# Kernel tuning notes

Hardware: AMD Instinct MI355X
Metric: run time of the kernel (lower is better)

## Reference

```python
import jax, jax.numpy as jnp
import numpy as np

BATCH, SEQ = 4, 2048
D_MODEL, INNER, STATE, K, FFN = 384, 768, 16, 4, 1024


def setup_inputs() -> dict:
    key = jax.random.key(0)
    ks = jax.random.split(key, 12)
    def g(k, shape, scale=0.02):
        return jax.random.normal(k, shape, jnp.float32) * scale
    return {
        "x": jax.random.normal(ks[0], (BATCH, SEQ, D_MODEL), jnp.float32),
        "rms1_w": jnp.ones((D_MODEL,), jnp.float32),
        "rms2_w": jnp.ones((D_MODEL,), jnp.float32),
        "in_proj_w": g(ks[1], (D_MODEL, 2 * INNER)),
        "conv_w": g(ks[2], (K, INNER, INNER)),
        "conv_b": jnp.zeros((INNER,), jnp.float32),
        "x_proj_w": g(ks[3], (INNER, 2 * STATE)),
        "dt_proj_w": g(ks[4], (INNER, INNER)),
        "dt_proj_b": jnp.zeros((INNER,), jnp.float32),
        "A_log": jnp.log(jax.random.uniform(ks[5], (INNER, STATE), jnp.float32, 1.0, 16.0)),
        "D_param": jnp.ones((INNER,), jnp.float32),
        "out_proj_w": g(ks[6], (INNER, D_MODEL)),
        "ln_gamma": jnp.ones((D_MODEL,), jnp.float32),
        "ln_beta": jnp.zeros((D_MODEL,), jnp.float32),
        "gate_w": g(ks[7], (D_MODEL, FFN)),
        "up_w": g(ks[8], (D_MODEL, FFN)),
        "down_w": g(ks[9], (FFN, D_MODEL)),
    }


def rms_norm(x, w, eps=1e-6):
    norm = jnp.sqrt(jnp.mean(jnp.square(x), axis=-1, keepdims=True) + eps)
    return x / norm * w


def layer_norm(x, gamma, beta, eps=1e-5):
    mu = jnp.mean(x, axis=-1, keepdims=True)
    var = jnp.mean(jnp.square(x - mu), axis=-1, keepdims=True)
    return (x - mu) / jnp.sqrt(var + eps) * gamma + beta


def selective_scan(x, delta, A_log, Bm, Cm, Dp):
    # x, delta: [B,L,Di]; Bm, Cm: [B,L,N]; A_log: [Di,N]; Dp: [Di]
    delta = jax.nn.softplus(delta)
    A = -jnp.exp(A_log)                          # [Di,N]
    A_disc = jnp.exp(delta[..., None] * A)       # [B,L,Di,N]
    B_disc = delta[..., None] * Bm[:, :, None, :]  # [B,L,Di,N]
    xs = jnp.moveaxis(x, 1, 0)       # [L,B,Di]
    As = jnp.moveaxis(A_disc, 1, 0)  # [L,B,Di,N]
    Bs = jnp.moveaxis(B_disc, 1, 0)  # [L,B,Di,N]
    Cs = jnp.moveaxis(Cm, 1, 0)      # [L,B,N]
    h0 = jnp.zeros((x.shape[0], A_log.shape[0], A_log.shape[1]), x.dtype)
    def step(h, inp):
        x_t, A_t, B_t, C_t = inp
        h = A_t * h + B_t * x_t[..., None]          # [B,Di,N]
        y_t = jnp.einsum('bdn,bn->bd', h, C_t)      # [B,Di]
        return h, y_t
    _, ys = jax.lax.scan(step, h0, (xs, As, Bs, Cs))
    y = jnp.moveaxis(ys, 0, 1)       # [B,L,Di]
    return y + Dp * x


def mamba_core(h, in_proj_w, conv_w, conv_b, x_proj_w, dt_proj_w, dt_proj_b,
               A_log, D_param, out_proj_w, ln_gamma, ln_beta):
    xz = h @ in_proj_w                             # [B,L,2*Di]
    x_inner, z = jnp.split(xz, 2, axis=-1)
    # Conv1D SAME padding (k=4 -> pad (1,2)), channels-last, kernel [W,I,O]
    x_conv = jax.lax.conv_general_dilated(
        x_inner, conv_w, window_strides=(1,), padding='SAME',
        dimension_numbers=('NWC', 'WIO', 'NWC')) + conv_b
    x_conv = jax.nn.silu(x_conv)
    Bm, Cm = jnp.split(x_conv @ x_proj_w, 2, axis=-1)  # each [B,L,N]
    delta = x_conv @ dt_proj_w + dt_proj_b            # [B,L,Di]
    y = selective_scan(x_conv, delta, A_log, Bm, Cm, D_param)
    y = y * jax.nn.silu(z)
    out = y @ out_proj_w
    return layer_norm(out, ln_gamma, ln_beta)


def reference(x, rms1_w, rms2_w, in_proj_w, conv_w, conv_b, x_proj_w,
              dt_proj_w, dt_proj_b, A_log, D_param, out_proj_w, ln_gamma,
              ln_beta, gate_w, up_w, down_w):
    residual = x
    h = rms_norm(x, rms1_w)
    h = mamba_core(h, in_proj_w, conv_w, conv_b, x_proj_w, dt_proj_w,
                   dt_proj_b, A_log, D_param, out_proj_w, ln_gamma, ln_beta)
    x = residual + h  # dropout inactive (training=False)
    residual = x
    h = rms_norm(x, rms2_w)
    hidden = jax.nn.silu(h @ gate_w) * (h @ up_w)
    x = residual + hidden @ down_w
    return x
```

## Files before the change

kernel.cpp:

```cpp
#include <hip/hip_runtime.h>
#include <hip/hip_bf16.h>


using u16 = unsigned short;
using u32 = unsigned int;
using short8 = __attribute__((ext_vector_type(8))) short;
using f32x4  = __attribute__((ext_vector_type(4))) float;

#define TTOK 8192
#define DM 384
#define DI 768
#define NST 16
#define LSEQ 2048
#define NCH 64
#define LCH 32

#define SWZ_R(row, quad) \
  ((row) * 32 + ((((quad) ^ (row) ^ ((row) >> 2)) & 3) * 8))
#define SWZ_W(tid) SWZ_R((tid) >> 2, (tid) & 3)

__device__ __forceinline__ float bf2f(u16 a) {
  u32 u = ((u32)a) << 16;
  float f; __builtin_memcpy(&f, &u, 4); return f;
}
__device__ __forceinline__ u16 f2bf(float f) {
  u32 u; __builtin_memcpy(&u, &f, 4);
  u32 r = (u + 0x7fffu + ((u >> 16) & 1u)) >> 16;
  return (u16)r;
}
__device__ __forceinline__ int probe_bf(const void* rw) {
  return (((const u32*)rw)[0] == 0x3F803F80u) ? 1 : 0;
}
__device__ __forceinline__ float ld_in(const void* p, int i, int isbf) {
  return isbf ? bf2f(((const u16*)p)[i]) : ((const float*)p)[i];
}
__device__ __forceinline__ float fexp2(float x) {
#if __has_builtin(__builtin_amdgcn_exp2f)
  return __builtin_amdgcn_exp2f(x);
#else
  return exp2f(x);
#endif
}
__device__ __forceinline__ float wave_sum(float v) {
#pragma unroll
  for (int off = 32; off > 0; off >>= 1) v += __shfl_xor(v, off, 64);
  return v;
}

__global__ __launch_bounds__(256) void k_prep(
    const void* __restrict__ in_proj, const void* __restrict__ conv_w,
    const void* __restrict__ dt_w, const void* __restrict__ x_proj,
    const void* __restrict__ out_proj, const void* __restrict__ gate_w,
    const void* __restrict__ up_w, const void* __restrict__ down_w,
    const void* __restrict__ A_log, const void* __restrict__ conv_b,
    const void* __restrict__ dt_b, const void* __restrict__ Dp,
    const void* __restrict__ rms1_w, const void* __restrict__ rms2_w,
    const void* __restrict__ gamma, const void* __restrict__ beta,
    u16* __restrict__ W1T, u16* __restrict__ WCT, u16* __restrict__ W45T,
    u16* __restrict__ W5T, u16* __restrict__ W6T, u16* __restrict__ W7T,
    float* __restrict__ An2T, u16* __restrict__ vecs,
    u16* __restrict__ WinX, u16* __restrict__ h1pad) {
  const int isbf = probe_bf(rms1_w);
  int idx = blockIdx.x * 256 + threadIdx.x;
#define XPOSE(base, n, src, dst, R, C)                         \
  if (idx < (base) + (n)) {                                    \
    int lo = idx - (base);                                     \
    int r = lo / (C), c = lo % (C);                            \
    dst[(size_t)c * (R) + r] = f2bf(ld_in(src, lo, isbf));     \
    return;                                                    \
  }
  XPOSE(0,       589824,  in_proj,  W1T, 384, 1536)
  if (idx < 2949120) {
    int lo = idx - 589824;
    int t = lo / 589824, rem = lo % 589824;
    int j = rem / 768, n = rem % 768;
    WCT[(size_t)t * 589824 + n * 768 + j] = f2bf(ld_in(conv_w, lo, isbf));
    return;
  }
  XPOSE(2949120, 589824,  dt_w,     W45T, 768, 768)
  XPOSE(3538944, 24576,   x_proj,  (W45T + (size_t)768 * 768), 768, 32)
  XPOSE(3563520, 294912,  out_proj, W5T, 768, 384)
  XPOSE(3858432, 393216,  gate_w,   W6T, 384, 1024)
  XPOSE(4251648, 393216,  up_w,    (W6T + (size_t)1024 * 384), 384, 1024)
  XPOSE(4644864, 393216,  down_w,   W7T, 1024, 384)
#undef XPOSE
  if (idx < 5332992) {
    int lo = idx - 5038080;
    int i = lo / 768, j = lo % 768;
    WinX[lo] = f2bf(ld_in(in_proj, i * 1536 + j, isbf));
    return;
  }
  if (idx < 5345280) {
    int lo = idx - 5332992;
    int d = lo >> 4, n = lo & 15;
    An2T[n * DI + d] = -__expf(ld_in(A_log, lo, isbf)) * 1.44269504f;
    return;
  }
  if (idx < 5349120) {
    int lo = idx - 5345280;
    const void* s; int o;
    if      (lo < 768)  { s = conv_b; o = lo; }
    else if (lo < 1536) { s = dt_b;   o = lo - 768; }
    else if (lo < 2304) { s = Dp;     o = lo - 1536; }
    else if (lo < 2688) { s = rms1_w; o = lo - 2304; }
    else if (lo < 3072) { s = rms2_w; o = lo - 2688; }
    else if (lo < 3456) { s = gamma;  o = lo - 3072; }
    else                { s = beta;   o = lo - 3456; }
    vecs[lo] = f2bf(ld_in(s, o, isbf));
    return;
  }
  if (idx < 5353728) {
    int lo = idx - 5349120;
    int b = lo / (3 * DM), rem = lo % (3 * DM);
    int which = rem / DM, i = rem % DM;
    int row = b * 2051 + (which == 0 ? 0 : (2048 + which));
    h1pad[(size_t)row * DM + i] = 0;
  }
}

#define V_CB 0
#define V_DB 768
#define V_DP 1536
#define V_R1 2304
#define V_R2 2688
#define V_GA 3072
#define V_BE 3456

__global__ __launch_bounds__(128) void k_rms1(const void* __restrict__ x,
                                              const void* __restrict__ rw,
                                              const u16* __restrict__ vecs,
                                              u16* __restrict__ h1pad) {
  const int isbf = probe_bf(rw);
  int t = blockIdx.x, tid = threadIdx.x;
  int lane = tid & 63, wid = tid >> 6;
  float v[3]; float q = 0.f;
#pragma unroll
  for (int j = 0; j < 3; ++j) {
    v[j] = ld_in(x, t * DM + tid + j * 128, isbf);
    q += v[j] * v[j];
  }
  q = wave_sum(q);
  __shared__ float rq[2];
  if (lane == 0) rq[wid] = q;
  __syncthreads();
  float rr = rsqrtf((rq[0] + rq[1]) * (1.f / DM) + 1e-6f);
  int b = t >> 11, l = t & 2047;
  size_t orow = ((size_t)(b * 2051 + l + 1)) * DM;
#pragma unroll
  for (int j = 0; j < 3; ++j) {
    int i = tid + j * 128;
    h1pad[orow + i] = f2bf(v[j] * rr * bf2f(vecs[V_R1 + i]));
  }
}

__global__ __launch_bounds__(128) void k_lnrms(const float* __restrict__ outm,
                                               const void* __restrict__ xin,
                                               const void* __restrict__ rw,
                                               const u16* __restrict__ vecs,
                                               float* __restrict__ x2f,
                                               u16* __restrict__ h2) {
  const int isbf = probe_bf(rw);
  int t = blockIdx.x, tid = threadIdx.x;
  int lane = tid & 63, wid = tid >> 6;
  float v[3]; float s = 0.f, q = 0.f;
#pragma unroll
  for (int j = 0; j < 3; ++j) {
    v[j] = outm[(size_t)t * DM + tid + j * 128];
    s += v[j]; q += v[j] * v[j];
  }
  s = wave_sum(s); q = wave_sum(q);
  __shared__ float rs[2], rq[2], r2[2];
  if (lane == 0) { rs[wid] = s; rq[wid] = q; }
  __syncthreads();
  float mu = (rs[0] + rs[1]) * (1.f / DM);
  float var = (rq[0] + rq[1]) * (1.f / DM) - mu * mu;
  float rstd = rsqrtf(var + 1e-5f);
  float x2v[3]; float q2 = 0.f;
#pragma unroll
  for (int j = 0; j < 3; ++j) {
    int i = tid + j * 128;
    float ln = (v[j] - mu) * rstd * bf2f(vecs[V_GA + i]) + bf2f(vecs[V_BE + i]);
    x2v[j] = ld_in(xin, t * DM + i, isbf) + ln;
    x2f[(size_t)t * DM + i] = x2v[j];
    q2 += x2v[j] * x2v[j];
  }
  q2 = wave_sum(q2);
  if (lane == 0) r2[wid] = q2;
  __syncthreads();
  float rr = rsqrtf((r2[0] + r2[1]) * (1.f / DM) + 1e-6f);
#pragma unroll
  for (int j = 0; j < 3; ++j) {
    int i = tid + j * 128;
    h2[(size_t)t * DM + i] = f2bf(x2v[j] * rr * bf2f(vecs[V_R2 + i]));
  }
}

template <int EPI, int MT, int KDIM>
__global__ __launch_bounds__(256) void gemm_bt(
    const u16* __restrict__ A, const u16* __restrict__ BT,
    float* __restrict__ o1, float* __restrict__ o2,
    u16* __restrict__ ob1, u16* __restrict__ ob2,
    const u16* __restrict__ bias, const float* __restrict__ res,
    const void* __restrict__ fl) {
  constexpr int AFR = MT / 32;
  __shared__ u16 smem[MT * 64 + 8192];
  const int tid = threadIdx.x;
  const int lane = tid & 63, wid = tid >> 6;
  const int wm = (wid >> 1) * (MT / 2), wn = (wid & 1) << 6;
  const int fr = lane & 15, quad = lane >> 4;
  const int r0 = tid >> 2, c8 = (tid & 3) << 3;
  const int m0 = blockIdx.x * MT, n0 = blockIdx.y * 128;

  f32x4 acc[AFR][4] = {};

  const u16* BTe = (EPI == 6) ? BT + (size_t)blockIdx.z * 589824 : BT;
  const u16* gB0 = BTe + (size_t)(n0 + r0) * KDIM + c8;
  const u16* gA0 = A + (size_t)(m0 + r0) * KDIM + c8;

  short8 a00, a01, a10, a11, b00, b01, b10, b11;
  auto stage_load = [&](int kt) {
    a00 = *(const short8*)(gA0 + kt);
    a10 = *(const short8*)(gA0 + kt + 32);
    if (MT == 128) {
      a01 = *(const short8*)(gA0 + kt + (size_t)64 * KDIM);
      a11 = *(const short8*)(gA0 + kt + 32 + (size_t)64 * KDIM);
    }
    b00 = *(const short8*)(gB0 + kt);
    b01 = *(const short8*)(gB0 + kt + (size_t)64 * KDIM);
    b10 = *(const short8*)(gB0 + kt + 32);
    b11 = *(const short8*)(gB0 + kt + 32 + (size_t)64 * KDIM);
  };

  stage_load(0);

#pragma unroll 1
  for (int kt = 0; kt < KDIM; kt += 64) {
    __syncthreads();
    *(short8*)&smem[SWZ_W(tid)] = a00;
    if (MT == 128) *(short8*)&smem[2048 + SWZ_W(tid)] = a01;
    *(short8*)&smem[MT * 32 + SWZ_W(tid)] = a10;
    if (MT == 128) *(short8*)&smem[MT * 32 + 2048 + SWZ_W(tid)] = a11;
    *(short8*)&smem[MT * 64 + SWZ_W(tid)]        = b00;
    *(short8*)&smem[MT * 64 + 2048 + SWZ_W(tid)] = b01;
    *(short8*)&smem[MT * 64 + 4096 + SWZ_W(tid)] = b10;
    *(short8*)&smem[MT * 64 + 6144 + SWZ_W(tid)] = b11;
    __syncthreads();
    if (kt + 64 < KDIM) stage_load(kt + 64);
#pragma unroll
    for (int kh = 0; kh < 2; ++kh) {
      const int ao = kh * MT * 32, bo = MT * 64 + kh * 4096;
      short8 af[AFR], bfg[4];
#pragma unroll
      for (int i = 0; i < AFR; ++i)
        af[i] = *(const short8*)&smem[ao + SWZ_R(wm + i * 16 + fr, quad)];
#pragma unroll
      for (int i = 0; i < 4; ++i)
        bfg[i] = *(const short8*)&smem[bo + SWZ_R(wn + i * 16 + fr, quad)];
#pragma unroll
      for (int mt = 0; mt < AFR; ++mt)
#pragma unroll
        for (int nt = 0; nt < 4; ++nt)
          acc[mt][nt] = __builtin_amdgcn_mfma_f32_16x16x32_bf16(
              af[mt], bfg[nt], acc[mt][nt], 0, 0, 0);
    }
  }

  int isbf = 0;
  if (EPI == 5) isbf = probe_bf(fl);

#pragma unroll
  for (int mt = 0; mt < AFR; ++mt) {
#pragma unroll
    for (int nt = 0; nt < 4; ++nt) {
#pragma unroll
      for (int r = 0; r < 4; ++r) {
        int t = m0 + wm + mt * 16 + quad * 4 + r;
        int n = n0 + wn + nt * 16 + fr;
        float v = acc[mt][nt][r];
        if (EPI == 2) {
          if (n < DI) {
            float xx = v + bf2f(bias[n]);
            float sp = (xx > 20.f) ? xx : log1pf(__expf(xx));
            ob1[(size_t)t * DI + n] = f2bf(sp);
          } else if (n < DI + 32) {
            o2[(size_t)t * 32 + (n - DI)] = v;
          }
        } else if (EPI == 3) {
          o1[(size_t)t * DM + n] = v;
        } else if (EPI == 5) {
          float val = v + res[(size_t)t * DM + n];
          if (isbf) ob1[(size_t)t * DM + n] = f2bf(val);
          else      o1[(size_t)t * DM + n] = val;
        } else if (EPI == 6) {
          ob1[(size_t)n * 1536 + blockIdx.z * 384 + t] = f2bf(v);
        }
      }
    }
  }
}

__global__ __launch_bounds__(256) void gemm_xz(
    const u16* __restrict__ A, const u16* __restrict__ WC,
    const u16* __restrict__ WZ, u16* __restrict__ xconv,
    u16* __restrict__ zbuf, const u16* __restrict__ bias) {
  __shared__ u16 smem[12288];
  const int tid = threadIdx.x;
  const int lane = tid & 63, wid = tid >> 6;
  const int wm = (wid >> 1) << 5, wn = (wid & 1) << 6;
  const int fr = lane & 15, quad = lane >> 4;
  const int r0 = tid >> 2, c8 = (tid & 3) << 3;
  const int yb = blockIdx.y;
  const bool isz = yb >= 6;
  const int kd = isz ? 384 : 1536;
  const u16* BT = isz ? WZ : WC;
  const int kldb = isz ? 384 : 1536;
  const int n0 = (isz ? yb - 6 : yb) * 128;
  const int m0 = blockIdx.x * 64;

  f32x4 acc[2][4] = {};

  const u16* gB0 = BT + (size_t)(n0 + r0) * kldb + c8;
  const int b = m0 >> 11, l0 = m0 & 2047;
  const u16* gA0 = A + (size_t)(b * 2051 + l0 + r0 + (isz ? 1 : 0)) * DM + c8;

  short8 a0, a1, b00, b01, b10, b11;
  int wconv = 0, i0 = 0;
  auto calcA = [&]() -> const u16* {
    const u16* p = gA0 + (size_t)wconv * DM + i0;
    i0 += 32;
    if (i0 == DM) { i0 = 0; ++wconv; }
    return p;
  };
  auto stage_load = [&](int kt) {
    a0 = *(const short8*)calcA();
    a1 = *(const short8*)calcA();
    b00 = *(const short8*)(gB0 + kt);
    b01 = *(const short8*)(gB0 + kt + (size_t)64 * kldb);
    b10 = *(const short8*)(gB0 + kt + 32);
    b11 = *(const short8*)(gB0 + kt + 32 + (size_t)64 * kldb);
  };

  stage_load(0);

#pragma unroll 1
  for (int kt = 0; kt < kd; kt += 64) {
    __syncthreads();
    *(short8*)&smem[SWZ_W(tid)]         = a0;
    *(short8*)&smem[2048 + SWZ_W(tid)]  = a1;
    *(short8*)&smem[4096 + SWZ_W(tid)]  = b00;
    *(short8*)&smem[6144 + SWZ_W(tid)]  = b01;
    *(short8*)&smem[8192 + SWZ_W(tid)]  = b10;
    *(short8*)&smem[10240 + SWZ_W(tid)] = b11;
    __syncthreads();
    if (kt + 64 < kd) stage_load(kt + 64);
#pragma unroll
    for (int kh = 0; kh < 2; ++kh) {
      const int ao = kh * 2048, bo = 4096 + kh * 4096;
      short8 af[2], bfg[4];
#pragma unroll
      for (int i = 0; i < 2; ++i)
        af[i] = *(const short8*)&smem[ao + SWZ_R(wm + i * 16 + fr, quad)];
#pragma unroll
      for (int i = 0; i < 4; ++i)
        bfg[i] = *(const short8*)&smem[bo + SWZ_R(wn + i * 16 + fr, quad)];
#pragma unroll
      for (int mt = 0; mt < 2; ++mt)
#pragma unroll
        for (int nt = 0; nt < 4; ++nt)
          acc[mt][nt] = __builtin_amdgcn_mfma_f32_16x16x32_bf16(
              af[mt], bfg[nt], acc[mt][nt], 0, 0, 0);
    }
  }

#pragma unroll
  for (int mt = 0; mt < 2; ++mt) {
#pragma unroll
    for (int nt = 0; nt < 4; ++nt) {
#pragma unroll
      for (int r = 0; r < 4; ++r) {
        int t = m0 + wm + mt * 16 + quad * 4 + r;
        int n = n0 + wn + nt * 16 + fr;
        float v = acc[mt][nt][r];
        if (isz) {
          zbuf[(size_t)t * DI + n] = f2bf(v);
        } else {
          float xx = v + bf2f(bias[n]);
          float sg = 1.f / (1.f + __expf(-xx));
          xconv[(size_t)t * DI + n] = f2bf(xx * sg);
        }
      }
    }
  }
}

__global__ __launch_bounds__(256) void gemm_gu(
    const u16* __restrict__ A, const u16* __restrict__ W6T,
    u16* __restrict__ hid) {
  __shared__ u16 smem[20480];
  const int tid = threadIdx.x;
  const int lane = tid & 63, wid = tid >> 6;
  const int wm = (wid >> 1) << 5, wn = (wid & 1) << 6;
  const int fr = lane & 15, quad = lane >> 4;
  const int r0 = tid >> 2, c8 = (tid & 3) << 3;
  const int m0 = blockIdx.x * 64, n0 = blockIdx.y * 128;

  f32x4 accg[2][4] = {}, accu[2][4] = {};

  const u16* gA0 = A + (size_t)(m0 + r0) * DM + c8;
  const u16* gG0 = W6T + (size_t)(n0 + r0) * DM + c8;
  const u16* gU0 = W6T + (size_t)(1024 + n0 + r0) * DM + c8;

  short8 a0, a1, g00, g01, g10, g11, u00, u01, u10, u11;
  auto stage_load = [&](int kt) {
    a0  = *(const short8*)(gA0 + kt);
    a1  = *(const short8*)(gA0 + kt + 32);
    g00 = *(const short8*)(gG0 + kt);
    g01 = *(const short8*)(gG0 + kt + (size_t)64 * DM);
    g10 = *(const short8*)(gG0 + kt + 32);
    g11 = *(const short8*)(gG0 + kt + 32 + (size_t)64 * DM);
    u00 = *(const short8*)(gU0 + kt);
    u01 = *(const short8*)(gU0 + kt + (size_t)64 * DM);
    u10 = *(const short8*)(gU0 + kt + 32);
    u11 = *(const short8*)(gU0 + kt + 32 + (size_t)64 * DM);
  };

  stage_load(0);

#pragma unroll 1
  for (int kt = 0; kt < DM; kt += 64) {
    __syncthreads();
    *(short8*)&smem[SWZ_W(tid)]          = a0;
    *(short8*)&smem[2048 + SWZ_W(tid)]   = a1;
    *(short8*)&smem[4096 + SWZ_W(tid)]   = g00;
    *(short8*)&smem[6144 + SWZ_W(tid)]   = g01;
    *(short8*)&smem[8192 + SWZ_W(tid)]   = g10;
    *(short8*)&smem[10240 + SWZ_W(tid)]  = g11;
    *(short8*)&smem[12288 + SWZ_W(tid)]  = u00;
    *(short8*)&smem[14336 + SWZ_W(tid)]  = u01;
    *(short8*)&smem[16384 + SWZ_W(tid)]  = u10;
    *(short8*)&smem[18432 + SWZ_W(tid)]  = u11;
    __syncthreads();
    if (kt + 64 < DM) stage_load(kt + 64);
#pragma unroll
    for (int kh = 0; kh < 2; ++kh) {
      const int ao = kh * 2048, go = 4096 + kh * 4096, uo = 12288 + kh * 4096;
      short8 af[2], bg[4], bu[4];
#pragma unroll
      for (int i = 0; i < 2; ++i)
        af[i] = *(const short8*)&smem[ao + SWZ_R(wm + i * 16 + fr, quad)];
#pragma unroll
      for (int i = 0; i < 4; ++i) {
        bg[i] = *(const short8*)&smem[go + SWZ_R(wn + i * 16 + fr, quad)];
        bu[i] = *(const short8*)&smem[uo + SWZ_R(wn + i * 16 + fr, quad)];
      }
#pragma unroll
      for (int mt = 0; mt < 2; ++mt)
#pragma unroll
        for (int nt = 0; nt < 4; ++nt) {
          accg[mt][nt] = __builtin_amdgcn_mfma_f32_16x16x32_bf16(
              af[mt], bg[nt], accg[mt][nt], 0, 0, 0);
          accu[mt][nt] = __builtin_amdgcn_mfma_f32_16x16x32_bf16(
              af[mt], bu[nt], accu[mt][nt], 0, 0, 0);
        }
    }
  }

#pragma unroll
  for (int mt = 0; mt < 2; ++mt) {
#pragma unroll
    for (int nt = 0; nt < 4; ++nt) {
#pragma unroll
      for (int r = 0; r < 4; ++r) {
        int t = m0 + wm + mt * 16 + quad * 4 + r;
        int n = n0 + wn + nt * 16 + fr;
        float g = accg[mt][nt][r];
        float u = accu[mt][nt][r];
        float sg = 1.f / (1.f + __expf(-g));
        hid[(size_t)t * 1024 + n] = f2bf(g * sg * u);
      }
    }
  }
}

__global__ __launch_bounds__(256) void k_scan1(
    const u16* __restrict__ deltab, const u16* __restrict__ xconv,
    const float* __restrict__ BC, const float* __restrict__ An2T,
    float* __restrict__ hlb, float* __restrict__ Pb) {
  int gid = blockIdx.x * 256 + threadIdx.x;
  int d = gid % DI, bc = gid / DI, c = bc & (NCH - 1), b = bc >> 6;
  float An[NST];
#pragma unroll
  for (int n = 0; n < NST; ++n) An[n] = An2T[n * DI + d];
  float h[NST], P[NST];
#pragma unroll
  for (int n = 0; n < NST; ++n) { h[n] = 0.f; P[n] = 1.f; }
  int row0 = b * LSEQ + c * LCH;
  float dt = bf2f(deltab[(size_t)row0 * DI + d]);
  float xv = bf2f(xconv[(size_t)row0 * DI + d]);
  float4 q[4];
  {
    const float4* q4 = (const float4*)(BC + (size_t)row0 * 32);
#pragma unroll
    for (int i = 0; i < 4; ++i) q[i] = q4[i];
  }
  for (int s = 0; s < LCH; ++s) {
    float dtc = dt, xvc = xv;
    float Bm[NST];
#pragma unroll
    for (int i = 0; i < 4; ++i) {
      Bm[4*i] = q[i].x; Bm[4*i+1] = q[i].y;
      Bm[4*i+2] = q[i].z; Bm[4*i+3] = q[i].w;
    }
    if (s + 1 < LCH) {
      int r2 = row0 + s + 1;
      dt = bf2f(deltab[(size_t)r2 * DI + d]);
      xv = bf2f(xconv[(size_t)r2 * DI + d]);
      const float4* q4 = (const float4*)(BC + (size_t)r2 * 32);
#pragma unroll
      for (int i = 0; i < 4; ++i) q[i] = q4[i];
    }
    float dxv = dtc * xvc;
#pragma unroll
    for (int n = 0; n < NST; ++n) {
      float a = fexp2(dtc * An[n]);
      h[n] = fmaf(a, h[n], dxv * Bm[n]);
      P[n] *= a;
    }
  }
  float4* ph = (float4*)(hlb + (size_t)gid * NST);
  float4* pp = (float4*)(Pb + (size_t)gid * NST);
#pragma unroll
  for (int i = 0; i < 4; ++i) {
    ph[i] = make_float4(h[4*i], h[4*i+1], h[4*i+2], h[4*i+3]);
    pp[i] = make_float4(P[4*i], P[4*i+1], P[4*i+2], P[4*i+3]);
  }
}

__global__ __launch_bounds__(256) void k_scan2(const float* __restrict__ hlb,
                                               const float* __restrict__ Pb,
                                               float* __restrict__ hin) {
  int gid = blockIdx.x * 256 + threadIdx.x;
  int n = gid & 15, bd = gid >> 4;
  int d = bd % DI, b = bd / DI;
  float H = 0.f;
  for (int c = 0; c < NCH; ++c) {
    size_t idx = ((size_t)((b * NCH + c) * DI + d)) * NST + n;
    hin[idx] = H;
    H = hlb[idx] + Pb[idx] * H;
  }
}

__global__ __launch_bounds__(256) void k_scan3(
    const u16* __restrict__ deltab, const u16* __restrict__ xconv,
    const float* __restrict__ BC, const float* __restrict__ An2T,
    const float* __restrict__ hinb, const u16* __restrict__ zb,
    const u16* __restrict__ vecs, u16* __restrict__ ys) {
  int gid = blockIdx.x * 256 + threadIdx.x;
  int d = gid % DI, bc = gid / DI, c = bc & (NCH - 1), b = bc >> 6;
  float An[NST];
#pragma unroll
  for (int n = 0; n < NST; ++n) An[n] = An2T[n * DI + d];
  float h[NST];
  {
    const float4* hp = (const float4*)(hinb + (size_t)gid * NST);
#pragma unroll
    for (int i = 0; i < 4; ++i) {
      float4 t = hp[i];
      h[4*i] = t.x; h[4*i+1] = t.y; h[4*i+2] = t.z; h[4*i+3] = t.w;
    }
  }
  float Dd = bf2f(vecs[V_DP + d]);
  int row0 = b * LSEQ + c * LCH;
  float dt = bf2f(deltab[(size_t)row0 * DI + d]);
  float xv = bf2f(xconv[(size_t)row0 * DI + d]);
  float zv = bf2f(zb[(size_t)row0 * DI + d]);
  float4 q[8];
  {
    const float4* q4 = (const float4*)(BC + (size_t)row0 * 32);
#pragma unroll
    for (int i = 0; i < 8; ++i) q[i] = q4[i];
  }
  for (int s = 0; s < LCH; ++s) {
    int row = row0 + s;
    float dtc = dt, xvc = xv, zvc = zv;
    float Bm[NST], Cm[NST];
#pragma unroll
    for (int i = 0; i < 4; ++i) {
      Bm[4*i] = q[i].x;   Bm[4*i+1] = q[i].y;
      Bm[4*i+2] = q[i].z; Bm[4*i+3] = q[i].w;
      Cm[4*i] = q[4+i].x;   Cm[4*i+1] = q[4+i].y;
      Cm[4*i+2] = q[4+i].z; Cm[4*i+3] = q[4+i].w;
    }
    if (s + 1 < LCH) {
      int r2 = row + 1;
      dt = bf2f(deltab[(size_t)r2 * DI + d]);
      xv = bf2f(xconv[(size_t)r2 * DI + d]);
      zv = bf2f(zb[(size_t)r2 * DI + d]);
      const float4* q4 = (const float4*)(BC + (size_t)r2 * 32);
#pragma unroll
      for (int i = 0; i < 8; ++i) q[i] = q4[i];
    }
    float dxv = dtc * xvc;
    float yp[4] = {0.f, 0.f, 0.f, 0.f};
#pragma unroll
    for (int n = 0; n < NST; ++n) {
      float a = fexp2(dtc * An[n]);
      h[n] = fmaf(a, h[n], dxv * Bm[n]);
      yp[n & 3] = fmaf(h[n], Cm[n], yp[n & 3]);
    }
    float y = (yp[0] + yp[1]) + (yp[2] + yp[3]);
    float sz = zvc / (1.f + __expf(-zvc));
    ys[(size_t)row * DI + d] = f2bf((y + Dd * xvc) * sz);
  }
}

extern "C" void kernel_launch(void* const* d_in, const int* in_sizes, int n_in,
                              void* d_out, int out_size, void* d_ws,
                              size_t ws_size, hipStream_t stream) {
  (void)in_sizes; (void)n_in; (void)out_size;
  const void* x        = d_in[0];
  const void* rms1_w   = d_in[1];
  const void* rms2_w   = d_in[2];
  const void* in_proj  = d_in[3];
  const void* conv_w   = d_in[4];
  const void* conv_b   = d_in[5];
  const void* x_proj   = d_in[6];
  const void* dt_w     = d_in[7];
  const void* dt_b     = d_in[8];
  const void* A_log    = d_in[9];
  const void* Dp       = d_in[10];
  const void* out_proj = d_in[11];
  const void* gamma    = d_in[12];
  const void* beta     = d_in[13];
  const void* gate_w   = d_in[14];
  const void* up_w     = d_in[15];
  const void* down_w   = d_in[16];

  char* ws = (char*)d_ws;
  size_t off = 0;
  auto alloc = [&](size_t bytes) -> void* {
    void* p = ws + off;
    off = (off + bytes + 255) & ~(size_t)255;
    return p;
  };
  u16*   W1T   = (u16*)alloc((size_t)1536 * 384 * 2);
  u16*   WCT   = (u16*)alloc((size_t)4 * 768 * 768 * 2);
  u16*   W45T  = (u16*)alloc((size_t)896 * 768 * 2);
  u16*   W5T   = (u16*)alloc((size_t)384 * 768 * 2);
  u16*   W6T   = (u16*)alloc((size_t)2048 * 384 * 2);
  u16*   W7T   = (u16*)alloc((size_t)384 * 1024 * 2);
  float* An2T  = (float*)alloc((size_t)16 * 768 * 4);
  u16*   vecs  = (u16*)alloc(3840 * 2);
  u16*   WinX  = (u16*)alloc((size_t)384 * 768 * 2);
  u16*   WcombT= (u16*)alloc((size_t)768 * 1536 * 2);
  u16*   h1pad = (u16*)alloc((size_t)4 * 2051 * 384 * 2);
  u16*   zbuf  = (u16*)alloc((size_t)8192 * 768 * 2);
  u16*   xconv = (u16*)alloc((size_t)8192 * 768 * 2);
  u16*   deltab= (u16*)alloc((size_t)8192 * 768 * 2);
  float* BCb   = (float*)alloc((size_t)8192 * 32 * 4);
  float* hl    = (float*)alloc((size_t)196608 * 16 * 4);
  float* Pb    = (float*)alloc((size_t)196608 * 16 * 4);
  float* hin   = (float*)alloc((size_t)196608 * 16 * 4);
  u16*   ys   = (u16*)hl;
  float* outm = Pb;
  float* x2f  = hin;
  u16*   h2   = h1pad;
  u16*   hid  = (u16*)hl;

  if (off > ws_size) return;

  k_prep<<<20913, 256, 0, stream>>>(
      in_proj, conv_w, dt_w, x_proj, out_proj, gate_w, up_w, down_w, A_log,
      conv_b, dt_b, Dp, rms1_w, rms2_w, gamma, beta,
      W1T, WCT, W45T, W5T, W6T, W7T, An2T, vecs, WinX, h1pad);

  gemm_bt<6, 128, 768><<<dim3(3, 6, 4), 256, 0, stream>>>(
      WinX, WCT, nullptr, nullptr, WcombT, nullptr, nullptr, nullptr, nullptr);

  k_rms1<<<8192, 128, 0, stream>>>(x, rms1_w, vecs, h1pad);

  gemm_xz<<<dim3(128, 12), 256, 0, stream>>>(
      h1pad, WcombT, W1T + (size_t)768 * 384, xconv, zbuf, vecs + V_CB);

  gemm_bt<2, 64, 768><<<dim3(128, 7), 256, 0, stream>>>(
      xconv, W45T, nullptr, BCb, deltab, nullptr, vecs + V_DB, nullptr,
      nullptr);

  k_scan1<<<768, 256, 0, stream>>>(deltab, xconv, BCb, An2T, hl, Pb);
  k_scan2<<<192, 256, 0, stream>>>(hl, Pb, hin);
  k_scan3<<<768, 256, 0, stream>>>(deltab, xconv, BCb, An2T, hin, zbuf, vecs,
                                   ys);

  gemm_bt<3, 64, 768><<<dim3(128, 3), 256, 0, stream>>>(
      ys, W5T, outm, nullptr, nullptr, nullptr, nullptr, nullptr, nullptr);
  k_lnrms<<<8192, 128, 0, stream>>>(outm, x, rms1_w, vecs, x2f, h2);

  gemm_gu<<<dim3(128, 8), 256, 0, stream>>>(h2, W6T, hid);
  gemm_bt<5, 64, 1024><<<dim3(128, 3), 256, 0, stream>>>(
      hid, W7T, (float*)d_out, nullptr, (u16*)d_out, nullptr, nullptr, x2f,
      rms1_w);
}
```

Baseline: 356.3 us.

## Tile weight transposes through LDS and fold RMSNorm1 into prep kernel

The weight-transposition part of the prep kernel now works on 64x64 tiles staged in shared memory, so both the reads and the writes are coalesced instead of strided per element. The first RMSNorm is merged into the same launch as extra blocks, each handling two tokens, which removes one kernel launch. The norm now reads rms1_w directly instead of the prepped vecs buffer, since that buffer is filled concurrently within the same launch. The grid shrinks and the block roles become more varied.

Measured after the change: 335.0 us. 6.0% less time.

```diff
diff --git a/kernel.cpp b/kernel.cpp
--- a/kernel.cpp
+++ b/kernel.cpp
@@ -47,77 +47,6 @@
   return v;
 }
 
-__global__ __launch_bounds__(256) void k_prep(
-    const void* __restrict__ in_proj, const void* __restrict__ conv_w,
-    const void* __restrict__ dt_w, const void* __restrict__ x_proj,
-    const void* __restrict__ out_proj, const void* __restrict__ gate_w,
-    const void* __restrict__ up_w, const void* __restrict__ down_w,
-    const void* __restrict__ A_log, const void* __restrict__ conv_b,
-    const void* __restrict__ dt_b, const void* __restrict__ Dp,
-    const void* __restrict__ rms1_w, const void* __restrict__ rms2_w,
-    const void* __restrict__ gamma, const void* __restrict__ beta,
-    u16* __restrict__ W1T, u16* __restrict__ WCT, u16* __restrict__ W45T,
-    u16* __restrict__ W5T, u16* __restrict__ W6T, u16* __restrict__ W7T,
-    float* __restrict__ An2T, u16* __restrict__ vecs,
-    u16* __restrict__ WinX, u16* __restrict__ h1pad) {
-  const int isbf = probe_bf(rms1_w);
-  int idx = blockIdx.x * 256 + threadIdx.x;
-#define XPOSE(base, n, src, dst, R, C)                         \
-  if (idx < (base) + (n)) {                                    \
-    int lo = idx - (base);                                     \
-    int r = lo / (C), c = lo % (C);                            \
-    dst[(size_t)c * (R) + r] = f2bf(ld_in(src, lo, isbf));     \
-    return;                                                    \
-  }
-  XPOSE(0,       589824,  in_proj,  W1T, 384, 1536)
-  if (idx < 2949120) {
-    int lo = idx - 589824;
-    int t = lo / 589824, rem = lo % 589824;
-    int j = rem / 768, n = rem % 768;
-    WCT[(size_t)t * 589824 + n * 768 + j] = f2bf(ld_in(conv_w, lo, isbf));
-    return;
-  }
-  XPOSE(2949120, 589824,  dt_w,     W45T, 768, 768)
-  XPOSE(3538944, 24576,   x_proj,  (W45T + (size_t)768 * 768), 768, 32)
-  XPOSE(3563520, 294912,  out_proj, W5T, 768, 384)
-  XPOSE(3858432, 393216,  gate_w,   W6T, 384, 1024)
-  XPOSE(4251648, 393216,  up_w,    (W6T + (size_t)1024 * 384), 384, 1024)
-  XPOSE(4644864, 393216,  down_w,   W7T, 1024, 384)
-#undef XPOSE
-  if (idx < 5332992) {
-    int lo = idx - 5038080;
-    int i = lo / 768, j = lo % 768;
-    WinX[lo] = f2bf(ld_in(in_proj, i * 1536 + j, isbf));
-    return;
-  }
-  if (idx < 5345280) {
-    int lo = idx - 5332992;
-    int d = lo >> 4, n = lo & 15;
-    An2T[n * DI + d] = -__expf(ld_in(A_log, lo, isbf)) * 1.44269504f;
-    return;
-  }
-  if (idx < 5349120) {
-    int lo = idx - 5345280;
-    const void* s; int o;
-    if      (lo < 768)  { s = conv_b; o = lo; }
-    else if (lo < 1536) { s = dt_b;   o = lo - 768; }
-    else if (lo < 2304) { s = Dp;     o = lo - 1536; }
-    else if (lo < 2688) { s = rms1_w; o = lo - 2304; }
-    else if (lo < 3072) { s = rms2_w; o = lo - 2688; }
-    else if (lo < 3456) { s = gamma;  o = lo - 3072; }
-    else                { s = beta;   o = lo - 3456; }
-    vecs[lo] = f2bf(ld_in(s, o, isbf));
-    return;
-  }
-  if (idx < 5353728) {
-    int lo = idx - 5349120;
-    int b = lo / (3 * DM), rem = lo % (3 * DM);
-    int which = rem / DM, i = rem % DM;
-    int row = b * 2051 + (which == 0 ? 0 : (2048 + which));
-    h1pad[(size_t)row * DM + i] = 0;
-  }
-}
-
 #define V_CB 0
 #define V_DB 768
 #define V_DP 1536
@@ -126,30 +55,119 @@
 #define V_GA 3072
 #define V_BE 3456
 
-__global__ __launch_bounds__(128) void k_rms1(const void* __restrict__ x,
-                                              const void* __restrict__ rw,
-                                              const u16* __restrict__ vecs,
-                                              u16* __restrict__ h1pad) {
-  const int isbf = probe_bf(rw);
-  int t = blockIdx.x, tid = threadIdx.x;
-  int lane = tid & 63, wid = tid >> 6;
-  float v[3]; float q = 0.f;
-#pragma unroll
-  for (int j = 0; j < 3; ++j) {
-    v[j] = ld_in(x, t * DM + tid + j * 128, isbf);
-    q += v[j] * v[j];
-  }
-  q = wave_sum(q);
-  __shared__ float rq[2];
-  if (lane == 0) rq[wid] = q;
-  __syncthreads();
-  float rr = rsqrtf((rq[0] + rq[1]) * (1.f / DM) + 1e-6f);
-  int b = t >> 11, l = t & 2047;
-  size_t orow = ((size_t)(b * 2051 + l + 1)) * DM;
-#pragma unroll
-  for (int j = 0; j < 3; ++j) {
-    int i = tid + j * 128;
-    h1pad[orow + i] = f2bf(v[j] * rr * bf2f(vecs[V_R1 + i]));
+__global__ __launch_bounds__(256) void k_prep(
+    const void* __restrict__ x, const void* __restrict__ in_proj,
+    const void* __restrict__ conv_w, const void* __restrict__ dt_w,
+    const void* __restrict__ x_proj, const void* __restrict__ out_proj,
+    const void* __restrict__ gate_w, const void* __restrict__ up_w,
+    const void* __restrict__ down_w, const void* __restrict__ A_log,
+    const void* __restrict__ conv_b, const void* __restrict__ dt_b,
+    const void* __restrict__ Dp, const void* __restrict__ rms1_w,
+    const void* __restrict__ rms2_w, const void* __restrict__ gamma,
+    const void* __restrict__ beta,
+    u16* __restrict__ W1T, u16* __restrict__ WCT, u16* __restrict__ W45T,
+    u16* __restrict__ W5T, u16* __restrict__ W6T, u16* __restrict__ W7T,
+    float* __restrict__ An2T, u16* __restrict__ vecs,
+    u16* __restrict__ WinX, u16* __restrict__ h1pad) {
+  const int isbf = probe_bf(rms1_w);
+  const int bx = blockIdx.x;
+  const int tid = threadIdx.x;
+  __shared__ u16 lt[64 * 66];
+
+  if (bx < 1236) {
+    const void* src; size_t soff = 0; u16* dst; int R, C, tpr, lo;
+    if (bx < 144)       { src = in_proj;  dst = W1T;  R = 384;  C = 1536; tpr = 24; lo = bx; }
+    else if (bx < 720)  { int tp = (bx - 144) / 144; lo = (bx - 144) % 144;
+                          src = conv_w; soff = (size_t)tp * 589824;
+                          dst = WCT + (size_t)tp * 589824; R = 768; C = 768; tpr = 12; }
+    else if (bx < 864)  { src = dt_w;     dst = W45T; R = 768;  C = 768;  tpr = 12; lo = bx - 720; }
+    else if (bx < 876)  { src = x_proj;   dst = W45T + (size_t)768 * 768;
+                          R = 768; C = 32; tpr = 1; lo = bx - 864; }
+    else if (bx < 948)  { src = out_proj; dst = W5T;  R = 768;  C = 384;  tpr = 6;  lo = bx - 876; }
+    else if (bx < 1044) { src = gate_w;   dst = W6T;  R = 384;  C = 1024; tpr = 16; lo = bx - 948; }
+    else if (bx < 1140) { src = up_w;     dst = W6T + (size_t)1024 * 384;
+                          R = 384; C = 1024; tpr = 16; lo = bx - 1044; }
+    else                { src = down_w;   dst = W7T;  R = 1024; C = 384;  tpr = 6;  lo = bx - 1140; }
+    int tr = lo / tpr, tc = lo % tpr;
+    int r0 = tr * 64, c0 = tc * 64;
+#pragma unroll
+    for (int i = 0; i < 16; ++i) {
+      int el = i * 256 + tid, lr = el >> 6, lc = el & 63;
+      if (c0 + lc < C)
+        lt[lr * 66 + lc] =
+            f2bf(ld_in(src, (int)(soff + (size_t)(r0 + lr) * C + c0 + lc), isbf));
+    }
+    __syncthreads();
+#pragma unroll
+    for (int i = 0; i < 16; ++i) {
+      int el = i * 256 + tid, orow = el >> 6, oc = el & 63;
+      if (c0 + orow < C)
+        dst[(size_t)(c0 + orow) * R + r0 + oc] = lt[oc * 66 + orow];
+    }
+    return;
+  }
+  if (bx < 5332) {
+    int half = tid >> 7;
+    int t = (bx - 1236) * 2 + half;
+    int tid2 = tid & 127;
+    int lane = tid & 63, wv = tid >> 6;
+    float v[3]; float q = 0.f;
+#pragma unroll
+    for (int j = 0; j < 3; ++j) {
+      v[j] = ld_in(x, t * DM + tid2 + j * 128, isbf);
+      q += v[j] * v[j];
+    }
+    q = wave_sum(q);
+    float* rq = (float*)lt;
+    if (lane == 0) rq[wv] = q;
+    __syncthreads();
+    float rr = rsqrtf((rq[half * 2] + rq[half * 2 + 1]) * (1.f / DM) + 1e-6f);
+    int b = t >> 11, l = t & 2047;
+    size_t orow = ((size_t)(b * 2051 + l + 1)) * DM;
+#pragma unroll
+    for (int j = 0; j < 3; ++j) {
+      int i = tid2 + j * 128;
+      h1pad[orow + i] = f2bf(v[j] * rr * ld_in(rms1_w, i, isbf));
+    }
+    return;
+  }
+  if (bx < 6484) {
+    int lo = (bx - 5332) * 256 + tid;
+    int i = lo / 768, j = lo % 768;
+    WinX[lo] = f2bf(ld_in(in_proj, i * 1536 + j, isbf));
+    return;
+  }
+  if (bx < 6532) {
+    int lo = (bx - 6484) * 256 + tid;
+    if (lo < 12288) {
+      int d = lo >> 4, n = lo & 15;
+      An2T[n * DI + d] = -__expf(ld_in(A_log, lo, isbf)) * 1.44269504f;
+    }
+    return;
+  }
+  if (bx < 6547) {
+    int lo = (bx - 6532) * 256 + tid;
+    if (lo < 3840) {
+      const void* s; int o;
+      if      (lo < 768)  { s = conv_b; o = lo; }
+      else if (lo < 1536) { s = dt_b;   o = lo - 768; }
+      else if (lo < 2304) { s = Dp;     o = lo - 1536; }
+      else if (lo < 2688) { s = rms1_w; o = lo - 2304; }
+      else if (lo < 3072) { s = rms2_w; o = lo - 2688; }
+      else if (lo < 3456) { s = gamma;  o = lo - 3072; }
+      else                { s = beta;   o = lo - 3456; }
+      vecs[lo] = f2bf(ld_in(s, o, isbf));
+    }
+    return;
+  }
+  {
+    int lo = (bx - 6547) * 256 + tid;
+    if (lo < 4608) {
+      int b = lo / (3 * DM), rem = lo % (3 * DM);
+      int which = rem / DM, i = rem % DM;
+      int row = b * 2051 + (which == 0 ? 0 : (2048 + which));
+      h1pad[(size_t)row * DM + i] = 0;
+    }
   }
 }
 
@@ -669,15 +687,13 @@
 
   if (off > ws_size) return;
 
-  k_prep<<<20913, 256, 0, stream>>>(
-      in_proj, conv_w, dt_w, x_proj, out_proj, gate_w, up_w, down_w, A_log,
-      conv_b, dt_b, Dp, rms1_w, rms2_w, gamma, beta,
+  k_prep<<<6565, 256, 0, stream>>>(
+      x, in_proj, conv_w, dt_w, x_proj, out_proj, gate_w, up_w, down_w,
+      A_log, conv_b, dt_b, Dp, rms1_w, rms2_w, gamma, beta,
       W1T, WCT, W45T, W5T, W6T, W7T, An2T, vecs, WinX, h1pad);
 
   gemm_bt<6, 128, 768><<<dim3(3, 6, 4), 256, 0, stream>>>(
       WinX, WCT, nullptr, nullptr, WcombT, nullptr, nullptr, nullptr, nullptr);
-
-  k_rms1<<<8192, 128, 0, stream>>>(x, rms1_w, vecs, h1pad);
 
   gemm_xz<<<dim3(128, 12), 256, 0, stream>>>(
       h1pad, WcombT, W1T + (size_t)768 * 384, xconv, zbuf, vecs + V_CB);
```
